# Kernel optimization log

Measured on AMD Instinct MI355X. Metric: run time of the kernel, lower is better.

## Reference

```python
import jax, jax.numpy as jnp
import numpy as np


def setup_inputs() -> dict:
    key = jax.random.key(0)
    ks = jax.random.split(key, 8)
    bs, slen, d = 16, 2048, 1024
    scale = 1.0 / np.sqrt(d)
    return {
        "query": jax.random.normal(ks[0], (bs, d), jnp.float32),
        "states": jax.random.normal(ks[1], (bs, slen, d), jnp.float32),
        "Wq": jax.random.normal(ks[2], (d, d), jnp.float32) * scale,
        "bq": jax.random.normal(ks[3], (d,), jnp.float32) * 0.01,
        "Wk": jax.random.normal(ks[4], (d, d), jnp.float32) * scale,
        "bk": jax.random.normal(ks[5], (d,), jnp.float32) * 0.01,
        "We": jax.random.normal(ks[6], (2 * d,), jnp.float32) * scale,
        "be": jax.random.normal(ks[7], (1,), jnp.float32) * 0.01,
    }


def reference(query, states, Wq, bq, Wk, bk, We, be):
    d = Wq.shape[1]
    # q: (bs, d); k: (bs, slen, d)
    q = jax.nn.relu(query @ Wq + bq)
    k = jax.nn.relu(jnp.einsum("bsv,vd->bsd", states, Wk) + bk)
    # tanh(cat(q, k)) @ We == tanh(q) @ We[:d] + tanh(k) @ We[d:]
    # (avoids materializing the repeated/concatenated (bs, slen, 2d) tensor)
    We_q, We_k = We[:d], We[d:]
    energy = (jnp.tanh(q) @ We_q)[:, None] + jnp.einsum("bsd,d->bs", jnp.tanh(k), We_k) + be[0]
    attn_weights = jax.nn.softmax(energy, axis=1)  # (bs, slen)
    attn = jnp.einsum("bs,bsd->bd", attn_weights, states)  # weighted sum of values
    return attn_weights, attn
```

## Files before the change

### kernel.cpp

```cpp
#include <hip/hip_runtime.h>
#include <hip/hip_bf16.h>

#define D 1024
#define SLEN 2048
#define BS 16
#define MROWS (BS*SLEN)

typedef __attribute__((ext_vector_type(8))) short short8;
typedef __attribute__((ext_vector_type(4))) float f32x4;

__device__ __forceinline__ short f2bf(float f) {
  __hip_bfloat16 h = __float2bfloat16(f);
  return __builtin_bit_cast(short, h);
}

__device__ __forceinline__ float4 ntload4(const float* p) {
  f32x4 v = __builtin_nontemporal_load((const f32x4*)p);
  float4 r; r.x = v.x; r.y = v.y; r.z = v.z; r.w = v.w; return r;
}

__global__ __launch_bounds__(256) void wk_prep(const float* __restrict__ Wk,
                                               short* __restrict__ WkT) {
  const int g = blockIdx.x;
  const int t = threadIdx.x;
#pragma unroll
  for (int it = 0; it < 4; ++it) {
    const int n = it*256 + t;
    short8 p;
#pragma unroll
    for (int j = 0; j < 8; ++j)
      p[j] = f2bf(Wk[(size_t)(g*8 + j)*D + n]);
    *(short8*)(WkT + ((size_t)g*D + n)*8) = p;
  }
}

__global__ __launch_bounds__(512, 2) void energy_gemm(
    const float* __restrict__ states, const short* __restrict__ WkT,
    const float* __restrict__ bk, const float* __restrict__ We,
    float* __restrict__ eraw)
{
  __shared__ short Al[64 * 129 * 8];

  const int tid  = threadIdx.x;
  const int w    = tid >> 6;
  const int lane = tid & 63;
  const int quad = lane >> 4;
  const int l16  = lane & 15;
  const int m0   = blockIdx.x * 64;

  {
    const int row = tid >> 3;
    const int u0  = tid & 7;
    const float* Ag = states + (size_t)(m0 + row)*D;
#pragma unroll
    for (int i = 0; i < 16; ++i) {
      const int u = u0 + i*8;
      float4 x0 = ntload4(Ag + u*8);
      float4 x1 = ntload4(Ag + u*8 + 4);
      short8 p;
      p[0]=f2bf(x0.x); p[1]=f2bf(x0.y); p[2]=f2bf(x0.z); p[3]=f2bf(x0.w);
      p[4]=f2bf(x1.x); p[5]=f2bf(x1.y); p[6]=f2bf(x1.z); p[7]=f2bf(x1.w);
      *(short8*)(Al + ((size_t)row*129 + u)*8) = p;
    }
  }
  __syncthreads();

  f32x4 acc[2][4][4];
#pragma unroll
  for (int nc = 0; nc < 2; ++nc)
#pragma unroll
    for (int mi = 0; mi < 4; ++mi)
#pragma unroll
      for (int ni = 0; ni < 4; ++ni)
        acc[nc][mi][ni] = (f32x4){0.f, 0.f, 0.f, 0.f};

  const short* bbase = WkT + ((size_t)quad*D + w*128 + l16)*8;
  const short* abase = Al + ((size_t)l16*129 + quad)*8;

#define LOADB(ks, buf)                                                   \
  {                                                                      \
    const short* bp = bbase + (size_t)(ks)*32768;                        \
    _Pragma("unroll")                                                    \
    for (int nc = 0; nc < 2; ++nc)                                       \
      _Pragma("unroll")                                                  \
      for (int ni = 0; ni < 4; ++ni)                                     \
        buf[nc*4 + ni] = *(const short8*)(bp + nc*512 + ni*128);         \
  }

#define LOADA(ks, buf)                                                   \
  {                                                                      \
    _Pragma("unroll")                                                    \
    for (int mi = 0; mi < 4; ++mi)                                       \
      buf[mi] = *(const short8*)(abase + mi*16512 + (ks)*32);            \
  }

#define MFMAS(fa, fb)                                                    \
  {                                                                      \
    _Pragma("unroll")                                                    \
    for (int nc = 0; nc < 2; ++nc)                                       \
      _Pragma("unroll")                                                  \
      for (int mi = 0; mi < 4; ++mi)                                     \
        _Pragma("unroll")                                                \
        for (int ni = 0; ni < 4; ++ni)                                   \
          acc[nc][mi][ni] = __builtin_amdgcn_mfma_f32_16x16x32_bf16(     \
              fa[mi], fb[nc*4 + ni], acc[nc][mi][ni], 0, 0, 0);          \
  }

  short8 fa0[4], fa1[4], fb0[8], fb1[8];
  LOADA(0, fa0); LOADB(0, fb0);
#pragma unroll
  for (int kk = 0; kk < 16; ++kk) {
    LOADA(2*kk + 1, fa1); LOADB(2*kk + 1, fb1);
    MFMAS(fa0, fb0);
    if (kk < 15) { LOADA(2*kk + 2, fa0); LOADB(2*kk + 2, fb0); }
    MFMAS(fa1, fb1);
  }

  float esum[16];
#pragma unroll
  for (int q = 0; q < 16; ++q) esum[q] = 0.f;
#pragma unroll
  for (int nc = 0; nc < 2; ++nc)
#pragma unroll
    for (int ni = 0; ni < 4; ++ni) {
      const int n = w*128 + nc*64 + ni*16 + l16;
      const float bkv = bk[n];
      const float wev = We[D + n];
#pragma unroll
      for (int mi = 0; mi < 4; ++mi)
#pragma unroll
        for (int r = 0; r < 4; ++r) {
          float x = acc[nc][mi][ni][r] + bkv;
          x = fmaxf(x, 0.f);
          float ex = __expf(2.f * x);
          float th = 1.f - 2.f/(ex + 1.f);
          esum[mi*4 + r] += th * wev;
        }
    }
#pragma unroll
  for (int dd = 1; dd < 16; dd <<= 1)
#pragma unroll
    for (int q = 0; q < 16; ++q)
      esum[q] += __shfl_xor(esum[q], dd, 64);

  __syncthreads();
  float* red = (float*)Al;
  if (l16 == 0) {
#pragma unroll
    for (int mi = 0; mi < 4; ++mi)
#pragma unroll
      for (int r = 0; r < 4; ++r)
        red[(mi*16 + quad*4 + r)*8 + w] = esum[mi*4 + r];
  }
  __syncthreads();
  if (tid < 64) {
    float s = 0.f;
#pragma unroll
    for (int wi = 0; wi < 8; ++wi) s += red[tid*8 + wi];
    eraw[m0 + tid] = s;
  }
#undef LOADB
#undef LOADA
#undef MFMAS
}

__global__ __launch_bounds__(256) void softmax_rows(
    const float* __restrict__ eraw, float* __restrict__ wts) {
  const int b = blockIdx.x, t = threadIdx.x;
  __shared__ float red[256];
  float v[8];
  float m = -1e30f;
#pragma unroll
  for (int j = 0; j < 8; ++j) {
    v[j] = eraw[(size_t)b*SLEN + j*256 + t];
    m = fmaxf(m, v[j]);
  }
  red[t] = m; __syncthreads();
  for (int s = 128; s > 0; s >>= 1) {
    if (t < s) red[t] = fmaxf(red[t], red[t+s]);
    __syncthreads();
  }
  m = red[0];
  __syncthreads();
  float sum = 0.f;
#pragma unroll
  for (int j = 0; j < 8; ++j) { v[j] = __expf(v[j] - m); sum += v[j]; }
  red[t] = sum; __syncthreads();
  for (int s = 128; s > 0; s >>= 1) {
    if (t < s) red[t] += red[t+s];
    __syncthreads();
  }
  const float inv = 1.f / red[0];
#pragma unroll
  for (int j = 0; j < 8; ++j)
    wts[(size_t)b*SLEN + j*256 + t] = v[j] * inv;
}

__global__ __launch_bounds__(256) void attn_partial(
    const float* __restrict__ states, const float* __restrict__ wts,
    float* __restrict__ part)
{
  const int sc = blockIdx.x;
  const int b  = blockIdx.y;
  const int t  = threadIdx.x;
  __shared__ float wsh[32];
  if (t < 32) wsh[t] = wts[(size_t)b*SLEN + sc*32 + t];
  __syncthreads();
  const float* sp = states + ((size_t)b*SLEN + sc*32)*D + t*4;
  float ax = 0.f, ay = 0.f, az = 0.f, aw = 0.f;
#pragma unroll
  for (int s = 0; s < 32; ++s) {
    float4 x = ntload4(sp + (size_t)s*D);
    const float wv = wsh[s];
    ax = fmaf(wv, x.x, ax);
    ay = fmaf(wv, x.y, ay);
    az = fmaf(wv, x.z, az);
    aw = fmaf(wv, x.w, aw);
  }
  float4 o; o.x = ax; o.y = ay; o.z = az; o.w = aw;
  *(float4*)(part + ((size_t)(b*64 + sc))*D + t*4) = o;
}

__global__ __launch_bounds__(256) void attn_final(
    const float* __restrict__ part, float* __restrict__ attn)
{
  const int b = blockIdx.x, t = threadIdx.x;
  float4 s = {0.f, 0.f, 0.f, 0.f};
#pragma unroll
  for (int sc = 0; sc < 64; ++sc) {
    float4 v = *(const float4*)(part + ((size_t)(b*64 + sc))*D + t*4);
    s.x += v.x; s.y += v.y; s.z += v.z; s.w += v.w;
  }
  *(float4*)(attn + (size_t)b*D + t*4) = s;
}

extern "C" void kernel_launch(void* const* d_in, const int* in_sizes, int n_in,
                              void* d_out, int out_size, void* d_ws, size_t ws_size,
                              hipStream_t stream) {
  const float* states = (const float*)d_in[1];
  const float* Wk     = (const float*)d_in[4];
  const float* bk     = (const float*)d_in[5];
  const float* We     = (const float*)d_in[6];
  float* out = (float*)d_out;

  short* WkT  = (short*)d_ws;
  float* eraw = (float*)((char*)d_ws + (size_t)D*D*sizeof(short));
  float* part = (float*)((char*)d_ws + (size_t)D*D*sizeof(short)
                                     + (size_t)MROWS*sizeof(float));

  (void)in_sizes; (void)n_in; (void)out_size; (void)ws_size;

  wk_prep<<<128, 256, 0, stream>>>(Wk, WkT);
  energy_gemm<<<MROWS/64, 512, 0, stream>>>(states, WkT, bk, We, eraw);
  softmax_rows<<<BS, 256, 0, stream>>>(eraw, out);
  attn_partial<<<dim3(64, BS), 256, 0, stream>>>(states, out, part);
  attn_final<<<BS, 256, 0, stream>>>(part, out + MROWS);
}
```

Baseline: 294.7 us.

## Pipeline states K-chunks through double-buffered LDS in larger energy GEMM tiles

The energy GEMM now takes 128-row tiles with 1024 threads and streams the states row slice in four 256-wide K chunks through a double-buffered LDS area. Each next chunk's global loads are issued before the MFMAs of the current chunk, so load latency can overlap with compute instead of staging the whole row first. Each wave covers 64 output columns over 8 M sub-tiles, which changes register pressure and the reuse of the Wk fragments. The attention pass also switches from nontemporal to regular loads of states, in the hope of hitting cache lines left behind by the GEMM.

```diff
diff --git a/kernel.cpp b/kernel.cpp
--- a/kernel.cpp
+++ b/kernel.cpp
@@ -19,6 +19,13 @@
   float4 r; r.x = v.x; r.y = v.y; r.z = v.z; r.w = v.w; return r;
 }
 
+__device__ __forceinline__ short8 pack8(const float4& a, const float4& b) {
+  short8 p;
+  p[0]=f2bf(a.x); p[1]=f2bf(a.y); p[2]=f2bf(a.z); p[3]=f2bf(a.w);
+  p[4]=f2bf(b.x); p[5]=f2bf(b.y); p[6]=f2bf(b.z); p[7]=f2bf(b.w);
+  return p;
+}
+
 __global__ __launch_bounds__(256) void wk_prep(const float* __restrict__ Wk,
                                                short* __restrict__ WkT) {
   const int g = blockIdx.x;
@@ -34,129 +41,144 @@
   }
 }
 
-__global__ __launch_bounds__(512, 2) void energy_gemm(
+__global__ __launch_bounds__(1024, 4) void energy_gemm(
     const float* __restrict__ states, const short* __restrict__ WkT,
     const float* __restrict__ bk, const float* __restrict__ We,
     float* __restrict__ eraw)
 {
-  __shared__ short Al[64 * 129 * 8];
+  __shared__ short Al[2][128*33*8];
 
   const int tid  = threadIdx.x;
   const int w    = tid >> 6;
   const int lane = tid & 63;
   const int quad = lane >> 4;
   const int l16  = lane & 15;
-  const int m0   = blockIdx.x * 64;
-
-  {
-    const int row = tid >> 3;
-    const int u0  = tid & 7;
-    const float* Ag = states + (size_t)(m0 + row)*D;
-#pragma unroll
-    for (int i = 0; i < 16; ++i) {
-      const int u = u0 + i*8;
-      float4 x0 = ntload4(Ag + u*8);
-      float4 x1 = ntload4(Ag + u*8 + 4);
-      short8 p;
-      p[0]=f2bf(x0.x); p[1]=f2bf(x0.y); p[2]=f2bf(x0.z); p[3]=f2bf(x0.w);
-      p[4]=f2bf(x1.x); p[5]=f2bf(x1.y); p[6]=f2bf(x1.z); p[7]=f2bf(x1.w);
-      *(short8*)(Al + ((size_t)row*129 + u)*8) = p;
-    }
-  }
-  __syncthreads();
-
-  f32x4 acc[2][4][4];
-#pragma unroll
-  for (int nc = 0; nc < 2; ++nc)
-#pragma unroll
-    for (int mi = 0; mi < 4; ++mi)
-#pragma unroll
-      for (int ni = 0; ni < 4; ++ni)
-        acc[nc][mi][ni] = (f32x4){0.f, 0.f, 0.f, 0.f};
-
-  const short* bbase = WkT + ((size_t)quad*D + w*128 + l16)*8;
-  const short* abase = Al + ((size_t)l16*129 + quad)*8;
-
-#define LOADB(ks, buf)                                                   \
+  const int m0   = blockIdx.x * 128;
+
+  const int srow = tid >> 3;
+  const int su0  = tid & 7;
+  const float* Ag = states + (size_t)(m0 + srow)*D + su0*8;
+  short* sdst = &Al[0][0];
+
+#pragma unroll
+  for (int i = 0; i < 4; ++i) {
+    float4 x0 = ntload4(Ag + i*64);
+    float4 x1 = ntload4(Ag + i*64 + 4);
+    *(short8*)(&Al[0][((size_t)srow*33 + su0 + i*8)*8]) = pack8(x0, x1);
+  }
+  __syncthreads();
+
+  f32x4 acc[8][4];
+#pragma unroll
+  for (int mi = 0; mi < 8; ++mi)
+#pragma unroll
+    for (int ni = 0; ni < 4; ++ni)
+      acc[mi][ni] = (f32x4){0.f, 0.f, 0.f, 0.f};
+
+  const short* bb = WkT + ((size_t)quad*D + w*64 + l16)*8;
+
+#define LOADB(kg, buf)                                                   \
   {                                                                      \
-    const short* bp = bbase + (size_t)(ks)*32768;                        \
+    const short* bp = bb + (size_t)(kg)*32768;                           \
     _Pragma("unroll")                                                    \
-    for (int nc = 0; nc < 2; ++nc)                                       \
-      _Pragma("unroll")                                                  \
-      for (int ni = 0; ni < 4; ++ni)                                     \
-        buf[nc*4 + ni] = *(const short8*)(bp + nc*512 + ni*128);         \
-  }
-
-#define LOADA(ks, buf)                                                   \
+    for (int ni = 0; ni < 4; ++ni)                                       \
+      buf[ni] = *(const short8*)(bp + ni*128);                           \
+  }
+
+#define LOADA(qb, ks, buf)                                               \
   {                                                                      \
+    const short* ap = &Al[qb][((size_t)l16*33 + quad)*8] + (ks)*32;      \
     _Pragma("unroll")                                                    \
-    for (int mi = 0; mi < 4; ++mi)                                       \
-      buf[mi] = *(const short8*)(abase + mi*16512 + (ks)*32);            \
+    for (int mi = 0; mi < 8; ++mi)                                       \
+      buf[mi] = *(const short8*)(ap + mi*4224);                          \
   }
 
 #define MFMAS(fa, fb)                                                    \
   {                                                                      \
     _Pragma("unroll")                                                    \
-    for (int nc = 0; nc < 2; ++nc)                                       \
+    for (int mi = 0; mi < 8; ++mi)                                       \
       _Pragma("unroll")                                                  \
-      for (int mi = 0; mi < 4; ++mi)                                     \
-        _Pragma("unroll")                                                \
-        for (int ni = 0; ni < 4; ++ni)                                   \
-          acc[nc][mi][ni] = __builtin_amdgcn_mfma_f32_16x16x32_bf16(     \
-              fa[mi], fb[nc*4 + ni], acc[nc][mi][ni], 0, 0, 0);          \
-  }
-
-  short8 fa0[4], fa1[4], fb0[8], fb1[8];
-  LOADA(0, fa0); LOADB(0, fb0);
-#pragma unroll
-  for (int kk = 0; kk < 16; ++kk) {
-    LOADA(2*kk + 1, fa1); LOADB(2*kk + 1, fb1);
-    MFMAS(fa0, fb0);
-    if (kk < 15) { LOADA(2*kk + 2, fa0); LOADB(2*kk + 2, fb0); }
-    MFMAS(fa1, fb1);
-  }
-
-  float esum[16];
-#pragma unroll
-  for (int q = 0; q < 16; ++q) esum[q] = 0.f;
-#pragma unroll
-  for (int nc = 0; nc < 2; ++nc)
-#pragma unroll
-    for (int ni = 0; ni < 4; ++ni) {
-      const int n = w*128 + nc*64 + ni*16 + l16;
-      const float bkv = bk[n];
-      const float wev = We[D + n];
-#pragma unroll
-      for (int mi = 0; mi < 4; ++mi)
-#pragma unroll
-        for (int r = 0; r < 4; ++r) {
-          float x = acc[nc][mi][ni][r] + bkv;
-          x = fmaxf(x, 0.f);
-          float ex = __expf(2.f * x);
-          float th = 1.f - 2.f/(ex + 1.f);
-          esum[mi*4 + r] += th * wev;
-        }
+      for (int ni = 0; ni < 4; ++ni)                                     \
+        acc[mi][ni] = __builtin_amdgcn_mfma_f32_16x16x32_bf16(           \
+            fa[mi], fb[ni], acc[mi][ni], 0, 0, 0);                       \
+  }
+
+  short8 fa[2][8], fb[2][4];
+  LOADB(0, fb[0]);
+
+#pragma unroll
+  for (int q = 0; q < 4; ++q) {
+    const int qb = q & 1, qn = qb ^ 1;
+
+    float4 sx[4][2];
+    if (q < 3) {
+#pragma unroll
+      for (int i = 0; i < 4; ++i) {
+        sx[i][0] = ntload4(Ag + (q+1)*256 + i*64);
+        sx[i][1] = ntload4(Ag + (q+1)*256 + i*64 + 4);
+      }
     }
+
+    LOADA(qb, 0, fa[0]);
+#pragma unroll
+    for (int ks = 0; ks < 8; ++ks) {
+      const int cur = ks & 1, nxt = cur ^ 1;
+      if (ks < 7) {
+        LOADA(qb, ks+1, fa[nxt]);
+        LOADB(q*8 + ks + 1, fb[nxt]);
+      } else if (q < 3) {
+        LOADB(q*8 + 8, fb[nxt]);
+      }
+      MFMAS(fa[cur], fb[cur]);
+    }
+
+    if (q < 3) {
+#pragma unroll
+      for (int i = 0; i < 4; ++i)
+        *(short8*)(&Al[qn][((size_t)srow*33 + su0 + i*8)*8]) = pack8(sx[i][0], sx[i][1]);
+      __syncthreads();
+    }
+  }
+
+  float esum[32];
+#pragma unroll
+  for (int qv = 0; qv < 32; ++qv) esum[qv] = 0.f;
+#pragma unroll
+  for (int ni = 0; ni < 4; ++ni) {
+    const int n = w*64 + ni*16 + l16;
+    const float bkv = bk[n];
+    const float wev = We[D + n];
+#pragma unroll
+    for (int mi = 0; mi < 8; ++mi)
+#pragma unroll
+      for (int r = 0; r < 4; ++r) {
+        float x = acc[mi][ni][r] + bkv;
+        x = fmaxf(x, 0.f);
+        float ex = __expf(2.f * x);
+        float th = 1.f - 2.f/(ex + 1.f);
+        esum[mi*4 + r] += th * wev;
+      }
+  }
 #pragma unroll
   for (int dd = 1; dd < 16; dd <<= 1)
 #pragma unroll
-    for (int q = 0; q < 16; ++q)
-      esum[q] += __shfl_xor(esum[q], dd, 64);
-
-  __syncthreads();
-  float* red = (float*)Al;
+    for (int qv = 0; qv < 32; ++qv)
+      esum[qv] += __shfl_xor(esum[qv], dd, 64);
+
+  __syncthreads();
+  float* red = (float*)&Al[0][0];
   if (l16 == 0) {
 #pragma unroll
-    for (int mi = 0; mi < 4; ++mi)
+    for (int mi = 0; mi < 8; ++mi)
 #pragma unroll
       for (int r = 0; r < 4; ++r)
-        red[(mi*16 + quad*4 + r)*8 + w] = esum[mi*4 + r];
-  }
-  __syncthreads();
-  if (tid < 64) {
+        red[(mi*16 + quad*4 + r)*16 + w] = esum[mi*4 + r];
+  }
+  __syncthreads();
+  if (tid < 128) {
     float s = 0.f;
 #pragma unroll
-    for (int wi = 0; wi < 8; ++wi) s += red[tid*8 + wi];
+    for (int wi = 0; wi < 16; ++wi) s += red[tid*16 + wi];
     eraw[m0 + tid] = s;
   }
 #undef LOADB
@@ -210,7 +232,7 @@
   float ax = 0.f, ay = 0.f, az = 0.f, aw = 0.f;
 #pragma unroll
   for (int s = 0; s < 32; ++s) {
-    float4 x = ntload4(sp + (size_t)s*D);
+    float4 x = *(const float4*)(sp + (size_t)s*D);
     const float wv = wsh[s];
     ax = fmaf(wv, x.x, ax);
     ay = fmaf(wv, x.y, ay);
@@ -251,7 +273,7 @@
   (void)in_sizes; (void)n_in; (void)out_size; (void)ws_size;
 
   wk_prep<<<128, 256, 0, stream>>>(Wk, WkT);
-  energy_gemm<<<MROWS/64, 512, 0, stream>>>(states, WkT, bk, We, eraw);
+  energy_gemm<<<MROWS/128, 1024, 0, stream>>>(states, WkT, bk, We, eraw);
   softmax_rows<<<BS, 256, 0, stream>>>(eraw, out);
   attn_partial<<<dim3(64, BS), 256, 0, stream>>>(states, out, part);
   attn_final<<<BS, 256, 0, stream>>>(part, out + MROWS);
```

Result: slower. 851.5 us (+188.9%).
